# Kernel tuning notes

Hardware: AMD Instinct MI355X
Metric: run time of the kernel (lower is better)

## Reference

```python
import jax, jax.numpy as jnp
import numpy as np

D = 128   # input_dim / num vars
LEAKY_SLOPE = 0.01  # torch F.leaky_relu default


def setup_inputs() -> dict:
    key = jax.random.key(0)
    ks = jax.random.split(key, 7)
    h, o, b = 64, 2, 8192
    scale = 0.05  # keep activations in a sane range
    return {
        "x": jax.random.normal(ks[0], (b, D), jnp.float32),
        "w0": jax.random.normal(ks[1], (D, h, D), jnp.float32) * scale,
        "w1": jax.random.normal(ks[2], (D, h, h), jnp.float32) * scale,
        "w2": jax.random.normal(ks[3], (D, o, h), jnp.float32) * scale,
        "b0": jax.random.normal(ks[4], (D, h), jnp.float32) * scale,
        "b1": jax.random.normal(ks[5], (D, h), jnp.float32) * scale,
        "b2": jax.random.normal(ks[6], (D, o), jnp.float32) * scale,
    }


def reference(x, w0, w1, w2, b0, b1, b2):
    # adjacency: all-ones minus identity (variable t cannot see itself)
    adj = jnp.ones((D, D), x.dtype) - jnp.eye(D, dtype=x.dtype)  # [j? no: (i,j)] symmetric
    # layer 0: out[b,t,i] = sum_j w0[t,i,j] * adj[j,t] * x[b,j]
    # mask the per-variable weights once, then a single contraction (no (t,i,j,b) intermediate)
    w0m = w0 * adj.T[:, None, :]            # (t,i,j); adj symmetric so adj[j,t]==adj[t,j]
    h = jnp.einsum('tij,bj->bti', w0m, x) + b0
    h = jax.nn.leaky_relu(h, LEAKY_SLOPE)
    # layer 1: per-variable dense
    h = jnp.einsum('tij,btj->bti', w1, h) + b1
    h = jax.nn.leaky_relu(h, LEAKY_SLOPE)
    # layer 2 (output, no nonlinearity)
    out = jnp.einsum('tij,btj->bti', w2, h) + b2  # (b, D, output_dim)
    # torch version returns torch.unbind(out, 1); stacked array carries same values
    return out
```

## Files before the change

### kernel.cpp

```cpp
#include <hip/hip_runtime.h>


typedef __bf16 bf16_t;
typedef __bf16 bf16x8 __attribute__((ext_vector_type(8)));
typedef float  f32x4  __attribute__((ext_vector_type(4)));

#define LEAKY 0.01f

#define XB_OFF   0u
#define W0B_OFF  (2048u*1024u)
#define W1B_OFF  (4096u*1024u)
#define W2B_OFF  (5120u*1024u)

__global__ __launch_bounds__(256)
void brickify(const float* __restrict__ x,  const float* __restrict__ w0,
              const float* __restrict__ w1, const float* __restrict__ w2,
              unsigned char* __restrict__ ws)
{
    const int wid  = blockIdx.x * 4 + (threadIdx.x >> 6);
    const int lane = threadIdx.x & 63;
    const int lr = lane & 15, lq = lane >> 4;

    float v[8];
    if (wid < 2048) {
        int bt = wid >> 5, rem = wid & 31, nt = rem >> 2, ks = rem & 3;
        const float* s = x + (size_t)(bt*128 + nt*16 + lr) * 128 + ks*32 + lq*8;
        const float4 a = *(const float4*)s, b = *(const float4*)(s + 4);
        v[0]=a.x; v[1]=a.y; v[2]=a.z; v[3]=a.w;
        v[4]=b.x; v[5]=b.y; v[6]=b.z; v[7]=b.w;
    } else if (wid < 4096) {
        int u = wid - 2048, t = u >> 4, rem = u & 15, it = rem >> 2, ks = rem & 3;
        int k0 = ks*32 + lq*8;
        const float* s = w0 + (size_t)(t*64 + it*16 + lr) * 128 + k0;
        const float4 a = *(const float4*)s, b = *(const float4*)(s + 4);
        v[0]=a.x; v[1]=a.y; v[2]=a.z; v[3]=a.w;
        v[4]=b.x; v[5]=b.y; v[6]=b.z; v[7]=b.w;
        #pragma unroll
        for (int j = 0; j < 8; ++j) if (k0 + j == t) v[j] = 0.f;
    } else if (wid < 5120) {
        int u = wid - 4096, t = u >> 3, rem = u & 7, it = rem >> 1, ks = rem & 1;
        const float* s = w1 + (size_t)(t*64 + it*16 + lr) * 64 + ks*32 + lq*8;
        const float4 a = *(const float4*)s, b = *(const float4*)(s + 4);
        v[0]=a.x; v[1]=a.y; v[2]=a.z; v[3]=a.w;
        v[4]=b.x; v[5]=b.y; v[6]=b.z; v[7]=b.w;
    } else {
        int u = wid - 5120, t = u >> 1, ks = u & 1;
        #pragma unroll
        for (int j = 0; j < 8; ++j) v[j] = 0.f;
        if (lr < 2) {
            const float* s = w2 + (size_t)(t*2 + lr) * 64 + ks*32 + lq*8;
            const float4 a = *(const float4*)s, b = *(const float4*)(s + 4);
            v[0]=a.x; v[1]=a.y; v[2]=a.z; v[3]=a.w;
            v[4]=b.x; v[5]=b.y; v[6]=b.z; v[7]=b.w;
        }
    }
    union { bf16_t h[8]; uint4 q; } pk;
    #pragma unroll
    for (int j = 0; j < 8; ++j) pk.h[j] = (bf16_t)v[j];
    ((uint4*)ws)[(size_t)wid * 64 + lane] = pk.q;
}

__global__ __launch_bounds__(256, 2)
void fused_mlp(const unsigned char* __restrict__ ws,
               const float* __restrict__ b0, const float* __restrict__ b1,
               const float* __restrict__ b2, float* __restrict__ out)
{
    __shared__ __align__(16) unsigned char hsm[16384];

    const int tid  = threadIdx.x;
    const int w    = tid >> 6;
    const int lane = tid & 63;
    const int lr = lane & 15, lq = lane >> 4;
    const int g  = blockIdx.x;
    const int t  = blockIdx.y;

    const unsigned char* w0p = ws + W0B_OFF + (size_t)t*16384 + lane*16;
    const unsigned char* w1p = ws + W1B_OFF + (size_t)t*8192  + lane*16;
    const unsigned char* w2p = ws + W2B_OFF + (size_t)t*2048  + lane*16;
    bf16x8 w0f[4][4], w1f[4][2], w2f[2];
    #pragma unroll
    for (int it = 0; it < 4; ++it)
        #pragma unroll
        for (int ks = 0; ks < 4; ++ks)
            w0f[it][ks] = *(const bf16x8*)(w0p + (it*4+ks)*1024);
    #pragma unroll
    for (int it = 0; it < 4; ++it)
        #pragma unroll
        for (int ks = 0; ks < 2; ++ks)
            w1f[it][ks] = *(const bf16x8*)(w1p + (it*2+ks)*1024);
    #pragma unroll
    for (int ks = 0; ks < 2; ++ks)
        w2f[ks] = *(const bf16x8*)(w2p + ks*1024);

    f32x4 b0q[4], b1q[4];
    #pragma unroll
    for (int it = 0; it < 4; ++it) {
        b0q[it] = *(const f32x4*)(b0 + t*64 + it*16 + lq*4);
        b1q[it] = *(const f32x4*)(b1 + t*64 + it*16 + lq*4);
    }
    const float2 b2v = *(const float2*)(b2 + t*2);

    const unsigned char* xp = ws + XB_OFF + lane*16;
    bf16x8 xf[2][4];
    {
        const int bt0 = g*8;
        #pragma unroll
        for (int ntl = 0; ntl < 2; ++ntl)
            #pragma unroll
            for (int ks = 0; ks < 4; ++ks)
                xf[ntl][ks] = *(const bf16x8*)(xp + (size_t)(((bt0*8 + w*2+ntl)*4 + ks))*1024);
    }

    for (int s = 0; s < 8; ++s) {
        const int bt = g*8 + s;

        f32x4 acc0[2][4];
        #pragma unroll
        for (int ntl = 0; ntl < 2; ++ntl)
            #pragma unroll
            for (int it = 0; it < 4; ++it) acc0[ntl][it] = b0q[it];

        #pragma unroll
        for (int ks = 0; ks < 4; ++ks)
            #pragma unroll
            for (int it = 0; it < 4; ++it)
                #pragma unroll
                for (int ntl = 0; ntl < 2; ++ntl)
                    acc0[ntl][it] = __builtin_amdgcn_mfma_f32_16x16x32_bf16(
                                        w0f[it][ks], xf[ntl][ks], acc0[ntl][it], 0, 0, 0);

        {
            const int btn = (s < 7) ? bt + 1 : bt;
            #pragma unroll
            for (int ntl = 0; ntl < 2; ++ntl)
                #pragma unroll
                for (int ks = 0; ks < 4; ++ks)
                    xf[ntl][ks] = *(const bf16x8*)(xp + (size_t)(((btn*8 + w*2+ntl)*4 + ks))*1024);
        }

        #pragma unroll
        for (int ntl = 0; ntl < 2; ++ntl)
            #pragma unroll
            for (int it = 0; it < 4; ++it) {
                union { bf16_t h[4]; unsigned long long u; } pk;
                #pragma unroll
                for (int r = 0; r < 4; ++r) {
                    float u = acc0[ntl][it][r];
                    pk.h[r] = (bf16_t)fmaxf(u, LEAKY * u);
                }
                int off = ((w*2+ntl)*2 + (it>>1)) * 1024
                        + (((it&1)*2 + (lq>>1))*16 + lr) * 16 + (lq&1)*8;
                *(unsigned long long*)(hsm + off) = pk.u;
            }

        bf16x8 hf[2][2];
        #pragma unroll
        for (int ntl = 0; ntl < 2; ++ntl)
            #pragma unroll
            for (int ks = 0; ks < 2; ++ks)
                hf[ntl][ks] = *(const bf16x8*)(hsm + ((w*2+ntl)*2 + ks)*1024 + lane*16);

        f32x4 acc1[2][4];
        #pragma unroll
        for (int ntl = 0; ntl < 2; ++ntl)
            #pragma unroll
            for (int it = 0; it < 4; ++it) acc1[ntl][it] = b1q[it];

        #pragma unroll
        for (int ks = 0; ks < 2; ++ks)
            #pragma unroll
            for (int it = 0; it < 4; ++it)
                #pragma unroll
                for (int ntl = 0; ntl < 2; ++ntl)
                    acc1[ntl][it] = __builtin_amdgcn_mfma_f32_16x16x32_bf16(
                                        w1f[it][ks], hf[ntl][ks], acc1[ntl][it], 0, 0, 0);

        #pragma unroll
        for (int ntl = 0; ntl < 2; ++ntl)
            #pragma unroll
            for (int it = 0; it < 4; ++it) {
                union { bf16_t h[4]; unsigned long long u; } pk;
                #pragma unroll
                for (int r = 0; r < 4; ++r) {
                    float u = acc1[ntl][it][r];
                    pk.h[r] = (bf16_t)fmaxf(u, LEAKY * u);
                }
                int off = ((w*2+ntl)*2 + (it>>1)) * 1024
                        + (((it&1)*2 + (lq>>1))*16 + lr) * 16 + (lq&1)*8;
                *(unsigned long long*)(hsm + off) = pk.u;
            }

        bf16x8 h2f[2][2];
        #pragma unroll
        for (int ntl = 0; ntl < 2; ++ntl)
            #pragma unroll
            for (int ks = 0; ks < 2; ++ks)
                h2f[ntl][ks] = *(const bf16x8*)(hsm + ((w*2+ntl)*2 + ks)*1024 + lane*16);

        f32x4 acc2[2];
        acc2[0] = (f32x4){0.f,0.f,0.f,0.f};
        acc2[1] = (f32x4){0.f,0.f,0.f,0.f};
        #pragma unroll
        for (int ks = 0; ks < 2; ++ks)
            #pragma unroll
            for (int ntl = 0; ntl < 2; ++ntl)
                acc2[ntl] = __builtin_amdgcn_mfma_f32_16x16x32_bf16(
                                w2f[ks], h2f[ntl][ks], acc2[ntl], 0, 0, 0);

        if (lq == 0) {
            #pragma unroll
            for (int ntl = 0; ntl < 2; ++ntl) {
                int row = bt*128 + (w*2+ntl)*16 + lr;
                float2 o2 = { acc2[ntl][0] + b2v.x, acc2[ntl][1] + b2v.y };
                *(float2*)(out + (size_t)row*256 + t*2) = o2;
            }
        }
    }
}

extern "C" void kernel_launch(void* const* d_in, const int* in_sizes, int n_in,
                              void* d_out, int out_size, void* d_ws, size_t ws_size,
                              hipStream_t stream) {
    const float* x  = (const float*)d_in[0];
    const float* w0 = (const float*)d_in[1];
    const float* w1 = (const float*)d_in[2];
    const float* w2 = (const float*)d_in[3];
    const float* b0 = (const float*)d_in[4];
    const float* b1 = (const float*)d_in[5];
    const float* b2 = (const float*)d_in[6];
    unsigned char* ws = (unsigned char*)d_ws;
    float* out = (float*)d_out;

    brickify<<<dim3(1344), dim3(256), 0, stream>>>(x, w0, w1, w2, ws);
    fused_mlp<<<dim3(8, 128), dim3(256), 0, stream>>>(ws, b0, b1, b2, out);
}
```

Baseline: 107.4 us.

## Split each block's batch tiles across 8 waves with one tile per wave

Blocks grow from 4 to 8 waves, and each wave now handles a single 16-row batch tile per step instead of two. This halves the per-wave accumulator and fragment registers and doubles the wave count available to hide MFMA and load latency. A second LDS buffer is added so the layer-1 and layer-2 activations use separate regions. The cost is that every wave redundantly holds the full per-variable weight fragments, so weight register and load cost per unit of work doubles, and MFMA independence per wave drops.

```diff
diff --git a/kernel.cpp b/kernel.cpp
--- a/kernel.cpp
+++ b/kernel.cpp
@@ -60,12 +60,13 @@
     ((uint4*)ws)[(size_t)wid * 64 + lane] = pk.q;
 }
 
-__global__ __launch_bounds__(256, 2)
+__global__ __launch_bounds__(512, 2)
 void fused_mlp(const unsigned char* __restrict__ ws,
                const float* __restrict__ b0, const float* __restrict__ b1,
                const float* __restrict__ b2, float* __restrict__ out)
 {
     __shared__ __align__(16) unsigned char hsm[16384];
+    __shared__ __align__(16) unsigned char h2sm[16384];
 
     const int tid  = threadIdx.x;
     const int w    = tid >> 6;
@@ -101,119 +102,88 @@
     const float2 b2v = *(const float2*)(b2 + t*2);
 
     const unsigned char* xp = ws + XB_OFF + lane*16;
-    bf16x8 xf[2][4];
-    {
-        const int bt0 = g*8;
-        #pragma unroll
-        for (int ntl = 0; ntl < 2; ++ntl)
-            #pragma unroll
-            for (int ks = 0; ks < 4; ++ks)
-                xf[ntl][ks] = *(const bf16x8*)(xp + (size_t)(((bt0*8 + w*2+ntl)*4 + ks))*1024);
-    }
+    bf16x8 xf[4];
+    #pragma unroll
+    for (int ks = 0; ks < 4; ++ks)
+        xf[ks] = *(const bf16x8*)(xp + (size_t)(((g*8 + 0)*8 + w)*4 + ks)*1024);
+
+    const int wboff = (((lq >> 1) * 16 + lr) * 16) + (lq & 1) * 8;
 
     for (int s = 0; s < 8; ++s) {
         const int bt = g*8 + s;
 
-        f32x4 acc0[2][4];
-        #pragma unroll
-        for (int ntl = 0; ntl < 2; ++ntl)
-            #pragma unroll
-            for (int it = 0; it < 4; ++it) acc0[ntl][it] = b0q[it];
+        f32x4 acc[4];
+        #pragma unroll
+        for (int it = 0; it < 4; ++it) acc[it] = b0q[it];
 
         #pragma unroll
         for (int ks = 0; ks < 4; ++ks)
             #pragma unroll
             for (int it = 0; it < 4; ++it)
-                #pragma unroll
-                for (int ntl = 0; ntl < 2; ++ntl)
-                    acc0[ntl][it] = __builtin_amdgcn_mfma_f32_16x16x32_bf16(
-                                        w0f[it][ks], xf[ntl][ks], acc0[ntl][it], 0, 0, 0);
+                acc[it] = __builtin_amdgcn_mfma_f32_16x16x32_bf16(
+                              w0f[it][ks], xf[ks], acc[it], 0, 0, 0);
 
         {
             const int btn = (s < 7) ? bt + 1 : bt;
             #pragma unroll
-            for (int ntl = 0; ntl < 2; ++ntl)
-                #pragma unroll
-                for (int ks = 0; ks < 4; ++ks)
-                    xf[ntl][ks] = *(const bf16x8*)(xp + (size_t)(((btn*8 + w*2+ntl)*4 + ks))*1024);
-        }
-
-        #pragma unroll
-        for (int ntl = 0; ntl < 2; ++ntl)
-            #pragma unroll
-            for (int it = 0; it < 4; ++it) {
-                union { bf16_t h[4]; unsigned long long u; } pk;
-                #pragma unroll
-                for (int r = 0; r < 4; ++r) {
-                    float u = acc0[ntl][it][r];
-                    pk.h[r] = (bf16_t)fmaxf(u, LEAKY * u);
-                }
-                int off = ((w*2+ntl)*2 + (it>>1)) * 1024
-                        + (((it&1)*2 + (lq>>1))*16 + lr) * 16 + (lq&1)*8;
-                *(unsigned long long*)(hsm + off) = pk.u;
+            for (int ks = 0; ks < 4; ++ks)
+                xf[ks] = *(const bf16x8*)(xp + (size_t)((btn*8 + w)*4 + ks)*1024);
+        }
+
+        #pragma unroll
+        for (int it = 0; it < 4; ++it) {
+            union { bf16_t h[4]; unsigned long long u; } pk;
+            #pragma unroll
+            for (int r = 0; r < 4; ++r) {
+                float u = acc[it][r];
+                pk.h[r] = (bf16_t)fmaxf(u, LEAKY * u);
             }
-
-        bf16x8 hf[2][2];
-        #pragma unroll
-        for (int ntl = 0; ntl < 2; ++ntl)
-            #pragma unroll
-            for (int ks = 0; ks < 2; ++ks)
-                hf[ntl][ks] = *(const bf16x8*)(hsm + ((w*2+ntl)*2 + ks)*1024 + lane*16);
-
-        f32x4 acc1[2][4];
-        #pragma unroll
-        for (int ntl = 0; ntl < 2; ++ntl)
-            #pragma unroll
-            for (int it = 0; it < 4; ++it) acc1[ntl][it] = b1q[it];
+            int off = (w*2 + (it>>1)) * 1024 + (it&1) * 512 + wboff;
+            *(unsigned long long*)(hsm + off) = pk.u;
+        }
+
+        bf16x8 hf[2];
+        #pragma unroll
+        for (int ks = 0; ks < 2; ++ks)
+            hf[ks] = *(const bf16x8*)(hsm + (w*2 + ks)*1024 + lane*16);
+
+        #pragma unroll
+        for (int it = 0; it < 4; ++it) acc[it] = b1q[it];
 
         #pragma unroll
         for (int ks = 0; ks < 2; ++ks)
             #pragma unroll
             for (int it = 0; it < 4; ++it)
-                #pragma unroll
-                for (int ntl = 0; ntl < 2; ++ntl)
-                    acc1[ntl][it] = __builtin_amdgcn_mfma_f32_16x16x32_bf16(
-                                        w1f[it][ks], hf[ntl][ks], acc1[ntl][it], 0, 0, 0);
-
-        #pragma unroll
-        for (int ntl = 0; ntl < 2; ++ntl)
-            #pragma unroll
-            for (int it = 0; it < 4; ++it) {
-                union { bf16_t h[4]; unsigned long long u; } pk;
-                #pragma unroll
-                for (int r = 0; r < 4; ++r) {
-                    float u = acc1[ntl][it][r];
-                    pk.h[r] = (bf16_t)fmaxf(u, LEAKY * u);
-                }
-                int off = ((w*2+ntl)*2 + (it>>1)) * 1024
-                        + (((it&1)*2 + (lq>>1))*16 + lr) * 16 + (lq&1)*8;
-                *(unsigned long long*)(hsm + off) = pk.u;
+                acc[it] = __builtin_amdgcn_mfma_f32_16x16x32_bf16(
+                              w1f[it][ks], hf[ks], acc[it], 0, 0, 0);
+
+        #pragma unroll
+        for (int it = 0; it < 4; ++it) {
+            union { bf16_t h[4]; unsigned long long u; } pk;
+            #pragma unroll
+            for (int r = 0; r < 4; ++r) {
+                float u = acc[it][r];
+                pk.h[r] = (bf16_t)fmaxf(u, LEAKY * u);
             }
-
-        bf16x8 h2f[2][2];
-        #pragma unroll
-        for (int ntl = 0; ntl < 2; ++ntl)
-            #pragma unroll
-            for (int ks = 0; ks < 2; ++ks)
-                h2f[ntl][ks] = *(const bf16x8*)(hsm + ((w*2+ntl)*2 + ks)*1024 + lane*16);
-
-        f32x4 acc2[2];
-        acc2[0] = (f32x4){0.f,0.f,0.f,0.f};
-        acc2[1] = (f32x4){0.f,0.f,0.f,0.f};
-        #pragma unroll
-        for (int ks = 0; ks < 2; ++ks)
-            #pragma unroll
-            for (int ntl = 0; ntl < 2; ++ntl)
-                acc2[ntl] = __builtin_amdgcn_mfma_f32_16x16x32_bf16(
-                                w2f[ks], h2f[ntl][ks], acc2[ntl], 0, 0, 0);
+            int off = (w*2 + (it>>1)) * 1024 + (it&1) * 512 + wboff;
+            *(unsigned long long*)(h2sm + off) = pk.u;
+        }
+
+        bf16x8 h2f[2];
+        #pragma unroll
+        for (int ks = 0; ks < 2; ++ks)
+            h2f[ks] = *(const bf16x8*)(h2sm + (w*2 + ks)*1024 + lane*16);
+
+        f32x4 acc2 = (f32x4){0.f, 0.f, 0.f, 0.f};
+        #pragma unroll
+        for (int ks = 0; ks < 2; ++ks)
+            acc2 = __builtin_amdgcn_mfma_f32_16x16x32_bf16(
+                       w2f[ks], h2f[ks], acc2, 0, 0, 0);
 
         if (lq == 0) {
-            #pragma unroll
-            for (int ntl = 0; ntl < 2; ++ntl) {
-                int row = bt*128 + (w*2+ntl)*16 + lr;
-                float2 o2 = { acc2[ntl][0] + b2v.x, acc2[ntl][1] + b2v.y };
-                *(float2*)(out + (size_t)row*256 + t*2) = o2;
-            }
+            int row = bt*128 + w*16 + lr;
+            float2 o2 = { acc2[0] + b2v.x, acc2[1] + b2v.y };
+            *(float2*)(out + (size_t)row*256 + t*2) = o2;
         }
     }
 }
@@ -232,5 +202,5 @@
     float* out = (float*)d_out;
 
     brickify<<<dim3(1344), dim3(256), 0, stream>>>(x, w0, w1, w2, ws);
-    fused_mlp<<<dim3(8, 128), dim3(256), 0, stream>>>(ws, b0, b1, b2, out);
+    fused_mlp<<<dim3(8, 128), dim3(512), 0, stream>>>(ws, b0, b1, b2, out);
 }
```

Measured after the change: 114.0 us. 1.06x slower.
